# Kernel optimization log

Measured on AMD Instinct MI355X. Metric: run time of the kernel, lower is better.

## Reference

```python
import jax, jax.numpy as jnp
import numpy as np


def _gru_cell(x, h, Wih, Whh, bih, bhh):
    # torch nn.GRU cell math: gates ordered [r, z, n]
    gi = Wih @ x + bih
    gh = Whh @ h + bhh
    ir, iz, inn = jnp.split(gi, 3)
    hr, hz, hn = jnp.split(gh, 3)
    r = jax.nn.sigmoid(ir + hr)
    z = jax.nn.sigmoid(iz + hz)
    n = jnp.tanh(inn + r * hn)
    return (1.0 - z) * n + z * h


def _lrelu(x):
    # torch nn.LeakyReLU default negative_slope=0.01
    return jnp.where(x >= 0, x, 0.01 * x)


def setup_inputs() -> dict:
    key = jax.random.key(0)
    ks = jax.random.split(key, 24)
    V, E, H, C, S, T = 32000, 512, 1024, 2048, 256, 129
    w = lambda k, shape: jax.random.normal(k, shape, jnp.float32) * 0.02
    return {
        "inputs": jax.random.randint(ks[0], (T,), 0, V),
        "h1": jax.random.normal(ks[1], (H,), jnp.float32),
        "h2": jax.random.normal(ks[2], (H,), jnp.float32),
        "projected_keys": jax.random.normal(ks[3], (S, H), jnp.float32),
        "encoder_outputs": jax.random.normal(ks[4], (S, C), jnp.float32),
        "embeds": jax.random.normal(ks[5], (V, E), jnp.float32),
        "Wq": w(ks[6], (H, H)),
        "v_att": w(ks[7], (H,)),
        "W_ih1": w(ks[8], (3 * H, E + C)),
        "W_hh1": w(ks[9], (3 * H, H)),
        "b_ih1": w(ks[10], (3 * H,)),
        "b_hh1": w(ks[11], (3 * H,)),
        "W_ih2": w(ks[12], (3 * H, H + C)),
        "W_hh2": w(ks[13], (3 * H, H)),
        "b_ih2": w(ks[14], (3 * H,)),
        "b_hh2": w(ks[15], (3 * H,)),
        "W_pre": w(ks[16], (H, E + H + C)),
        "b_pre": w(ks[17], (H,)),
        "W_out": w(ks[18], (E, H)),
        "b_out": w(ks[19], (E,)),
    }


def reference(inputs, h1, h2, projected_keys, encoder_outputs, embeds, Wq, v_att,
              W_ih1, W_hh1, b_ih1, b_hh1, W_ih2, W_hh2, b_ih2, b_hh2,
              W_pre, b_pre, W_out, b_out):
    # teacher_forcing = 1.0 -> decoder input at step i is inputs[i] (ground truth)
    emb_seq = embeds[inputs[:-1]]  # [T-1, E]

    def step(carry, emb):
        h1, h2 = carry
        # additive attention: query from top-layer hidden state
        q = Wq @ h2                                     # [H]
        e = jnp.tanh(projected_keys + q) @ v_att        # [S]
        alphas = jax.nn.softmax(e)                      # [S]
        context = alphas @ encoder_outputs              # [C]
        h1n = _gru_cell(jnp.concatenate([emb, context]), h1, W_ih1, W_hh1, b_ih1, b_hh1)
        o1 = _lrelu(h1n)                                # dropout identity (eval)
        h2n = _gru_cell(jnp.concatenate([o1, context]), h2, W_ih2, W_hh2, b_ih2, b_hh2)
        o2 = _lrelu(h2n)
        pre = _lrelu(W_pre @ jnp.concatenate([emb, o2, context]) + b_pre)  # [H]
        out = W_out @ o2 + b_out                        # [E]
        return (h1n, h2n), (out, pre, alphas)

    (h1f, h2f), (outs, pres, alphas) = jax.lax.scan(step, (h1, h2), emb_seq)
    # torch.cat(outputs, dim=1) of [1,1,E] pieces -> [1, T-1, E]
    return outs[None], pres[None], alphas, h1f, h2f
```

## Files before the change

kernel.cpp:

```cpp
#include <hip/hip_runtime.h>
#include <hip/hip_bf16.h>

typedef unsigned int uint32;
typedef unsigned short ushort16;

#define GBLK 256
#define BT 512
#define NSTEP 128

#define OFF_WQ    0ull
#define OFF_WHH1  1048576ull
#define OFF_WHH2  4194304ull
#define OFF_WIH1  7340032ull
#define OFF_WIH2  15204352ull
#define OFF_WPRE  24641536ull
#define OFF_WOUT  28311552ull
#define OFF_PK    28835840ull
#define OFF_ENC   29097984ull
#define CONV_TOTAL 29622272ull

struct Params {
  const int* inputs;
  const float *h1_in, *h2_in, *embeds, *vatt;
  const void *pk, *enc, *Wq, *Wih1, *Whh1, *Wih2, *Whh2, *Wpre, *Wout;
  const float *bih1, *bhh1, *bih2, *bhh2, *bpre, *bout;
  float* out;
  float* ws;
  int* bar;
  int cw;
};

__device__ __forceinline__ float blo(uint32 u) { return __uint_as_float(u << 16); }
__device__ __forceinline__ float bhi(uint32 u) { return __uint_as_float(u & 0xffff0000u); }
__device__ __forceinline__ uint32 bfr(float f) {
  uint32 u = __float_as_uint(f);
  return (u + 0x7fffu + ((u >> 16) & 1u)) >> 16;
}

__device__ __forceinline__ float ald(const float* a) {
  return __hip_atomic_load(a, __ATOMIC_RELAXED, __HIP_MEMORY_SCOPE_AGENT);
}
__device__ __forceinline__ void ast(float* a, float v) {
  __hip_atomic_store(a, v, __ATOMIC_RELAXED, __HIP_MEMORY_SCOPE_AGENT);
}

__device__ __forceinline__ float wsum(float v) {
#pragma unroll
  for (int o = 32; o; o >>= 1) v += __shfl_xor(v, o, 64);
  return v;
}

template <bool CW>
__device__ __forceinline__ float rowchunk(const void* W, size_t base, const float* xc, int lane) {
  const float* x = xc + lane * 8;
  float4 x0 = *(const float4*)x, x1 = *(const float4*)(x + 4);
  if constexpr (CW) {
    uint4 w = *(const uint4*)((const ushort16*)W + base + lane * 8);
    return blo(w.x) * x0.x + bhi(w.x) * x0.y + blo(w.y) * x0.z + bhi(w.y) * x0.w +
           blo(w.z) * x1.x + bhi(w.z) * x1.y + blo(w.w) * x1.z + bhi(w.w) * x1.w;
  } else {
    const float* wf = (const float*)W + base + lane * 8;
    float4 w0 = *(const float4*)wf, w1 = *(const float4*)(wf + 4);
    return w0.x * x0.x + w0.y * x0.y + w0.z * x0.z + w0.w * x0.w +
           w1.x * x1.x + w1.y * x1.y + w1.z * x1.z + w1.w * x1.w;
  }
}

template <bool CW, int K>
__device__ __forceinline__ float rowdot(const void* W, size_t rowbase, const float* x, int lane) {
  float s = 0.f;
#pragma unroll
  for (int c = 0; c < K; c += 512) s += rowchunk<CW>(W, rowbase + c, x + c, lane);
  return wsum(s);
}

__device__ __forceinline__ void gbar(int* bar, int k) {
  __syncthreads();
  if (threadIdx.x == 0) {
    const int grp = blockIdx.x >> 4;
    int* gcnt = bar + grp * 32;
    int* grel = bar + 512 + grp * 32;
    int* rcnt = bar + 1024;
    int* rrel = bar + 1056;
    int v = __hip_atomic_fetch_add(gcnt, 1, __ATOMIC_RELEASE, __HIP_MEMORY_SCOPE_AGENT);
    if (v == k * 16 - 1) {
      int r = __hip_atomic_fetch_add(rcnt, 1, __ATOMIC_RELEASE, __HIP_MEMORY_SCOPE_AGENT);
      if (r == k * 16 - 1)
        __hip_atomic_store(rrel, k, __ATOMIC_RELAXED, __HIP_MEMORY_SCOPE_AGENT);
      while (__hip_atomic_load(rrel, __ATOMIC_RELAXED, __HIP_MEMORY_SCOPE_AGENT) < k)
        __builtin_amdgcn_s_sleep(1);
      __hip_atomic_store(grel, k, __ATOMIC_RELAXED, __HIP_MEMORY_SCOPE_AGENT);
    } else {
      while (__hip_atomic_load(grel, __ATOMIC_RELAXED, __HIP_MEMORY_SCOPE_AGENT) < k)
        __builtin_amdgcn_s_sleep(1);
    }
  }
  __syncthreads();
}

__device__ __forceinline__ float sigm(float x) { return 1.f / (1.f + expf(-x)); }
__device__ __forceinline__ float lrelu(float x) { return x >= 0.f ? x : 0.01f * x; }

__device__ __forceinline__ void conv_arr(const float* src, ushort16* dst, int n, int g) {
  for (int i = g * 4; i < n; i += GBLK * BT * 4) {
    float4 v = *(const float4*)(src + i);
    uint2 o;
    o.x = bfr(v.x) | (bfr(v.y) << 16);
    o.y = bfr(v.z) | (bfr(v.w) << 16);
    *(uint2*)(dst + i) = o;
  }
}

template <bool CW>
__device__ void run_decoder(const Params& p, float* sx, float* s_red, float* s_part) {
  const int tid = threadIdx.x;
  const int lane = tid & 63;
  const int w = tid >> 6;
  const int b = blockIdx.x;
  const int gw = b * 8 + w;

  float* h1w = p.ws + 2048;
  float* h2w = p.ws + 3072;
  float* qw = p.ws + 4096;
  float* evw = p.ws + 5120;
  float* ctxw = p.ws + 5376;
  float* o1w = p.ws + 7424;
  float* o2w = p.ws + 8448;
  float* gh1 = p.ws + 9472;
  float* gh2 = p.ws + 12544;

  ushort16* cb = (ushort16*)((char*)p.ws + 65536);
  const void* Wqc = CW ? (const void*)(cb + OFF_WQ) : p.Wq;
  const void* Whh1c = CW ? (const void*)(cb + OFF_WHH1) : p.Whh1;
  const void* Whh2c = CW ? (const void*)(cb + OFF_WHH2) : p.Whh2;
  const void* Wih1c = CW ? (const void*)(cb + OFF_WIH1) : p.Wih1;
  const void* Wih2c = CW ? (const void*)(cb + OFF_WIH2) : p.Wih2;
  const void* Wprec = CW ? (const void*)(cb + OFF_WPRE) : p.Wpre;
  const void* Woutc = CW ? (const void*)(cb + OFF_WOUT) : p.Wout;
  const void* pkc = CW ? (const void*)(cb + OFF_PK) : p.pk;
  const void* encc = CW ? (const void*)(cb + OFF_ENC) : p.enc;

  float* outs = p.out;
  float* pres = p.out + 65536;
  float* alph = p.out + 196608;
  float* h1f = p.out + 229376;
  float* h2f = p.out + 230400;

  if constexpr (CW) {
    const int g = b * BT + tid;
    conv_arr((const float*)p.Wq, cb + OFF_WQ, 1048576, g);
    conv_arr((const float*)p.Whh1, cb + OFF_WHH1, 3145728, g);
    conv_arr((const float*)p.Whh2, cb + OFF_WHH2, 3145728, g);
    conv_arr((const float*)p.Wih1, cb + OFF_WIH1, 7864320, g);
    conv_arr((const float*)p.Wih2, cb + OFF_WIH2, 9437184, g);
    conv_arr((const float*)p.Wpre, cb + OFF_WPRE, 3670016, g);
    conv_arr((const float*)p.Wout, cb + OFF_WOUT, 524288, g);
    conv_arr((const float*)p.pk, cb + OFF_PK, 262144, g);
    conv_arr((const float*)p.enc, cb + OFF_ENC, 524288, g);
  }
  if (gw < 16) ast(h1w + gw * 64 + lane, p.h1_in[gw * 64 + lane]);
  else if (gw < 32) ast(h2w + (gw - 16) * 64 + lane, p.h2_in[(gw - 16) * 64 + lane]);

  int bk = 0;
  gbar(p.bar, ++bk);

  for (int t = 0; t <= NSTEP; ++t) {
    gbar(p.bar, ++bk);
    {
      const float* embp = p.embeds + (size_t)p.inputs[t > 0 ? t - 1 : 0] * 512;
      for (int i = tid; i < 5632; i += BT) {
        float v;
        if (i < 512) v = embp[i];
        else if (i < 1536) v = ald(o2w + i - 512);
        else if (i < 3584) v = ald(ctxw + i - 1536);
        else if (i < 4608) v = ald(h1w + i - 3584);
        else v = ald(h2w + i - 4608);
        sx[i] = v;
      }
      __syncthreads();
      if (gw < 1024) {
        if (t > 0) {
          float s = rowdot<CW, 3584>(Wprec, (size_t)gw * 3584, sx, lane);
          if (lane == 0) pres[(size_t)(t - 1) * 1024 + gw] = lrelu(s + p.bpre[gw]);
        }
        for (int j = gw; j < 2048; j += 1024) {
          float s = rowdot<CW, 1024>(Whh1c, (size_t)j * 1024, sx + 3584, lane);
          if (lane == 0) ast(gh1 + j, s + p.bhh1[j]);
        }
      } else {
        for (int j = 2048 + (gw - 1024); j < 7680; j += 1024) {
          if (j < 3072) {
            float s = rowdot<CW, 1024>(Whh1c, (size_t)j * 1024, sx + 3584, lane);
            if (lane == 0) ast(gh1 + j, s + p.bhh1[j]);
          } else if (j < 6144) {
            int r = j - 3072;
            float s = rowdot<CW, 1024>(Whh2c, (size_t)r * 1024, sx + 4608, lane);
            if (lane == 0) ast(gh2 + r, s + p.bhh2[r]);
          } else if (j < 7168) {
            int r = j - 6144;
            float s = rowdot<CW, 1024>(Wqc, (size_t)r * 1024, sx + 4608, lane);
            if (lane == 0) ast(qw + r, s);
          } else if (t > 0) {
            int r = j - 7168;
            float s = rowdot<CW, 1024>(Woutc, (size_t)r * 1024, sx + 512, lane);
            if (lane == 0) outs[(size_t)(t - 1) * 512 + r] = s + p.bout[r];
          }
        }
      }
    }
    if (t == NSTEP) break;

    gbar(p.bar, ++bk);
    if (w == 0) {
      const int base = lane * 16;
      float pkv[16], qv[16], vv[16];
      if constexpr (CW) {
        const uint4* pp = (const uint4*)((const ushort16*)pkc + (size_t)b * 1024 + base);
        uint4 a = pp[0], c = pp[1];
        pkv[0] = blo(a.x); pkv[1] = bhi(a.x); pkv[2] = blo(a.y); pkv[3] = bhi(a.y);
        pkv[4] = blo(a.z); pkv[5] = bhi(a.z); pkv[6] = blo(a.w); pkv[7] = bhi(a.w);
        pkv[8] = blo(c.x); pkv[9] = bhi(c.x); pkv[10] = blo(c.y); pkv[11] = bhi(c.y);
        pkv[12] = blo(c.z); pkv[13] = bhi(c.z); pkv[14] = blo(c.w); pkv[15] = bhi(c.w);
      } else {
#pragma unroll
        for (int k = 0; k < 4; ++k)
          *(float4*)(pkv + k * 4) = *(const float4*)((const float*)pkc + (size_t)b * 1024 + base + k * 4);
      }
#pragma unroll
      for (int k = 0; k < 16; ++k) qv[k] = ald(qw + base + k);
#pragma unroll
      for (int k = 0; k < 4; ++k)
        *(float4*)(vv + k * 4) = *(const float4*)(p.vatt + base + k * 4);
      float acc = 0.f;
#pragma unroll
      for (int k = 0; k < 16; ++k) acc += tanhf(pkv[k] + qv[k]) * vv[k];
      acc = wsum(acc);
      if (lane == 0) ast(evw + b, acc);
    }

    gbar(p.bar, ++bk);
    {
      float e_i = 0.f, pe = 0.f;
      if (tid < 256) {
        e_i = ald(evw + tid);
        float mw = e_i;
#pragma unroll
        for (int o = 32; o; o >>= 1) mw = fmaxf(mw, __shfl_xor(mw, o, 64));
        if (lane == 0) s_red[w] = mw;
      }
      __syncthreads();
      float m = fmaxf(fmaxf(s_red[0], s_red[1]), fmaxf(s_red[2], s_red[3]));
      __syncthreads();
      if (tid < 256) {
        pe = expf(e_i - m);
        float zw = wsum(pe);
        if (lane == 0) s_red[w] = zw;
      }
      __syncthreads();
      float Z = s_red[0] + s_red[1] + s_red[2] + s_red[3];
      const int j0 = b * 8;
      if (tid < 256) {
        float alpha = pe / Z;
        if (b == 0) alph[(size_t)t * 256 + tid] = alpha;
        float c[8];
        if constexpr (CW) {
          uint4 wv = *(const uint4*)((const ushort16*)encc + (size_t)tid * 2048 + j0);
          c[0] = blo(wv.x); c[1] = bhi(wv.x); c[2] = blo(wv.y); c[3] = bhi(wv.y);
          c[4] = blo(wv.z); c[5] = bhi(wv.z); c[6] = blo(wv.w); c[7] = bhi(wv.w);
        } else {
          const float* er = (const float*)encc + (size_t)tid * 2048 + j0;
          *(float4*)c = *(const float4*)er;
          *(float4*)(c + 4) = *(const float4*)(er + 4);
        }
#pragma unroll
        for (int j = 0; j < 8; ++j) sx[tid * 8 + j] = alpha * c[j];
      }
      __syncthreads();
      for (int st = 128; st >= 1; st >>= 1) {
        if (tid < st) {
#pragma unroll
          for (int j = 0; j < 8; ++j) sx[tid * 8 + j] += sx[(tid + st) * 8 + j];
        }
        __syncthreads();
      }
      if (tid < 8) ast(ctxw + j0 + tid, sx[tid]);
    }

    gbar(p.bar, ++bk);
    {
      const float* embc = p.embeds + (size_t)p.inputs[t] * 512;
      for (int i = tid; i < 2560; i += BT)
        sx[i] = (i < 512) ? embc[i] : ald(ctxw + i - 512);
      __syncthreads();
      const int i0 = b * 4;
      for (int mm = w; mm < 60; mm += 8) {
        int r = mm / 15, m = mm % 15;
        int g = m / 5, c = m % 5;
        int row = g * 1024 + i0 + r;
        float s = rowchunk<CW>(Wih1c, (size_t)row * 2560 + c * 512, sx + c * 512, lane);
        s = wsum(s);
        if (lane == 0) s_part[mm] = s;
      }
      __syncthreads();
      if (tid < 4) {
        const int i = i0 + tid;
        const float* sp = s_part + tid * 15;
        float sr = sp[0] + sp[1] + sp[2] + sp[3] + sp[4];
        float sz = sp[5] + sp[6] + sp[7] + sp[8] + sp[9];
        float sn = sp[10] + sp[11] + sp[12] + sp[13] + sp[14];
        float r = sigm(sr + p.bih1[i] + ald(gh1 + i));
        float z = sigm(sz + p.bih1[1024 + i] + ald(gh1 + 1024 + i));
        float n = tanhf(sn + p.bih1[2048 + i] + r * ald(gh1 + 2048 + i));
        float h = (1.f - z) * n + z * ald(h1w + i);
        ast(h1w + i, h);
        ast(o1w + i, lrelu(h));
      }
    }

    gbar(p.bar, ++bk);
    {
      for (int i = tid; i < 3072; i += BT)
        sx[i] = (i < 1024) ? ald(o1w + i) : ald(ctxw + i - 1024);
      __syncthreads();
      const int i0 = b * 4;
      for (int mm = w; mm < 72; mm += 8) {
        int r = mm / 18, m = mm % 18;
        int g = m / 6, c = m % 6;
        int row = g * 1024 + i0 + r;
        float s = rowchunk<CW>(Wih2c, (size_t)row * 3072 + c * 512, sx + c * 512, lane);
        s = wsum(s);
        if (lane == 0) s_part[mm] = s;
      }
      __syncthreads();
      if (tid < 4) {
        const int i = i0 + tid;
        const float* sp = s_part + tid * 18;
        float sr = sp[0] + sp[1] + sp[2] + sp[3] + sp[4] + sp[5];
        float sz = sp[6] + sp[7] + sp[8] + sp[9] + sp[10] + sp[11];
        float sn = sp[12] + sp[13] + sp[14] + sp[15] + sp[16] + sp[17];
        float r = sigm(sr + p.bih2[i] + ald(gh2 + i));
        float z = sigm(sz + p.bih2[1024 + i] + ald(gh2 + 1024 + i));
        float n = tanhf(sn + p.bih2[2048 + i] + r * ald(gh2 + 2048 + i));
        float h = (1.f - z) * n + z * ald(h2w + i);
        ast(h2w + i, h);
        ast(o2w + i, lrelu(h));
      }
    }
  }
  if (gw < 16) h1f[gw * 64 + lane] = ald(h1w + gw * 64 + lane);
  else if (gw < 32) h2f[(gw - 16) * 64 + lane] = ald(h2w + (gw - 16) * 64 + lane);
}

__global__ __launch_bounds__(BT, 2) void dec_SAVE_30683246363209_kernel(Params p) {
  __shared__ float sx[5632];
  __shared__ float s_red[8];
  __shared__ float s_part[72];
  if (p.cw) run_decoder<true>(p, sx, s_red, s_part);
  else run_decoder<false>(p, sx, s_red, s_part);
}

extern "C" void kernel_launch(void* const* d_in, const int* in_sizes, int n_in,
                              void* d_out, int out_size, void* d_ws, size_t ws_size,
                              hipStream_t stream) {
  hipMemsetAsync(d_ws, 0, 65536, stream);

  Params p;
  p.inputs = (const int*)d_in[0];
  p.h1_in = (const float*)d_in[1];
  p.h2_in = (const float*)d_in[2];
  p.pk = d_in[3];
  p.enc = d_in[4];
  p.embeds = (const float*)d_in[5];
  p.Wq = d_in[6];
  p.vatt = (const float*)d_in[7];
  p.Wih1 = d_in[8];
  p.Whh1 = d_in[9];
  p.bih1 = (const float*)d_in[10];
  p.bhh1 = (const float*)d_in[11];
  p.Wih2 = d_in[12];
  p.Whh2 = d_in[13];
  p.bih2 = (const float*)d_in[14];
  p.bhh2 = (const float*)d_in[15];
  p.Wpre = d_in[16];
  p.bpre = (const float*)d_in[17];
  p.Wout = d_in[18];
  p.bout = (const float*)d_in[19];
  p.out = (float*)d_out;
  p.ws = (float*)d_ws;
  p.bar = (int*)d_ws;
  p.cw = (ws_size >= (size_t)(65536 + CONV_TOTAL * 2)) ? 1 : 0;

  void* args[] = {&p};
  hipError_t err = hipLaunchCooperativeKernel((const void*)dec_SAVE_30683246363209_kernel,
                                              dim3(GBLK), dim3(BT), args, 0, stream);
  if (err != hipSuccess) {
    dec_SAVE_30683246363209_kernel<<<dim3(GBLK), dim3(BT), 0, stream>>>(p);
  }
}
```

Measured before the change: 6.865 ms.

## Keep all weights resident in registers as packed bf16 across decoder steps

Drops the global bf16 conversion pass into workspace. Each wave now loads its fixed weight rows once, converts them to packed bf16 and keeps them in registers (about 120 dwords per thread) for all 129 steps. The aim is to remove the per-step weight streaming from HBM/L2 that dominated each timestep. The attention energy is also spread across the whole block with an 8-wave reduction instead of running on one wave. The cost is heavy register pressure at 512 threads with 2 blocks per CU, which risks spills or losing occupancy, and the cooperative launch needs every block resident.

```diff
diff --git a/kernel.cpp b/kernel.cpp
--- a/kernel.cpp
+++ b/kernel.cpp
@@ -1,33 +1,19 @@
 #include <hip/hip_runtime.h>
-#include <hip/hip_bf16.h>
 
 typedef unsigned int uint32;
-typedef unsigned short ushort16;
 
 #define GBLK 256
 #define BT 512
 #define NSTEP 128
 
-#define OFF_WQ    0ull
-#define OFF_WHH1  1048576ull
-#define OFF_WHH2  4194304ull
-#define OFF_WIH1  7340032ull
-#define OFF_WIH2  15204352ull
-#define OFF_WPRE  24641536ull
-#define OFF_WOUT  28311552ull
-#define OFF_PK    28835840ull
-#define OFF_ENC   29097984ull
-#define CONV_TOTAL 29622272ull
-
 struct Params {
   const int* inputs;
   const float *h1_in, *h2_in, *embeds, *vatt;
-  const void *pk, *enc, *Wq, *Wih1, *Whh1, *Wih2, *Whh2, *Wpre, *Wout;
+  const float *pk, *enc, *Wq, *Wih1, *Whh1, *Wih2, *Whh2, *Wpre, *Wout;
   const float *bih1, *bhh1, *bih2, *bhh2, *bpre, *bout;
   float* out;
   float* ws;
   int* bar;
-  int cw;
 };
 
 __device__ __forceinline__ float blo(uint32 u) { return __uint_as_float(u << 16); }
@@ -50,28 +36,21 @@
   return v;
 }
 
-template <bool CW>
-__device__ __forceinline__ float rowchunk(const void* W, size_t base, const float* xc, int lane) {
+__device__ __forceinline__ void ldchunk(const float* W, size_t base, int lane, uint32* r) {
+  const float* wf = W + base + lane * 8;
+  float4 a = *(const float4*)wf;
+  float4 c = *(const float4*)(wf + 4);
+  r[0] = bfr(a.x) | (bfr(a.y) << 16);
+  r[1] = bfr(a.z) | (bfr(a.w) << 16);
+  r[2] = bfr(c.x) | (bfr(c.y) << 16);
+  r[3] = bfr(c.z) | (bfr(c.w) << 16);
+}
+
+__device__ __forceinline__ float dotchunk(const uint32* r, const float* xc, int lane) {
   const float* x = xc + lane * 8;
   float4 x0 = *(const float4*)x, x1 = *(const float4*)(x + 4);
-  if constexpr (CW) {
-    uint4 w = *(const uint4*)((const ushort16*)W + base + lane * 8);
-    return blo(w.x) * x0.x + bhi(w.x) * x0.y + blo(w.y) * x0.z + bhi(w.y) * x0.w +
-           blo(w.z) * x1.x + bhi(w.z) * x1.y + blo(w.w) * x1.z + bhi(w.w) * x1.w;
-  } else {
-    const float* wf = (const float*)W + base + lane * 8;
-    float4 w0 = *(const float4*)wf, w1 = *(const float4*)(wf + 4);
-    return w0.x * x0.x + w0.y * x0.y + w0.z * x0.z + w0.w * x0.w +
-           w1.x * x1.x + w1.y * x1.y + w1.z * x1.z + w1.w * x1.w;
-  }
-}
-
-template <bool CW, int K>
-__device__ __forceinline__ float rowdot(const void* W, size_t rowbase, const float* x, int lane) {
-  float s = 0.f;
-#pragma unroll
-  for (int c = 0; c < K; c += 512) s += rowchunk<CW>(W, rowbase + c, x + c, lane);
-  return wsum(s);
+  return blo(r[0]) * x0.x + bhi(r[0]) * x0.y + blo(r[1]) * x0.z + bhi(r[1]) * x0.w +
+         blo(r[2]) * x1.x + bhi(r[2]) * x1.y + blo(r[3]) * x1.z + bhi(r[3]) * x1.w;
 }
 
 __device__ __forceinline__ void gbar(int* bar, int k) {
@@ -101,23 +80,18 @@
 __device__ __forceinline__ float sigm(float x) { return 1.f / (1.f + expf(-x)); }
 __device__ __forceinline__ float lrelu(float x) { return x >= 0.f ? x : 0.01f * x; }
 
-__device__ __forceinline__ void conv_arr(const float* src, ushort16* dst, int n, int g) {
-  for (int i = g * 4; i < n; i += GBLK * BT * 4) {
-    float4 v = *(const float4*)(src + i);
-    uint2 o;
-    o.x = bfr(v.x) | (bfr(v.y) << 16);
-    o.y = bfr(v.z) | (bfr(v.w) << 16);
-    *(uint2*)(dst + i) = o;
-  }
-}
-
-template <bool CW>
-__device__ void run_decoder(const Params& p, float* sx, float* s_red, float* s_part) {
+__global__ __launch_bounds__(BT, 2) void dec_regw_kernel(Params p) {
+  __shared__ float sx[5632];
+  __shared__ float s_red[8];
+  __shared__ float s_part[72];
+
   const int tid = threadIdx.x;
   const int lane = tid & 63;
   const int w = tid >> 6;
   const int b = blockIdx.x;
   const int gw = b * 8 + w;
+  const int i0 = b * 4;
+  const int j0 = b * 8;
 
   float* h1w = p.ws + 2048;
   float* h2w = p.ws + 3072;
@@ -129,35 +103,71 @@
   float* gh1 = p.ws + 9472;
   float* gh2 = p.ws + 12544;
 
-  ushort16* cb = (ushort16*)((char*)p.ws + 65536);
-  const void* Wqc = CW ? (const void*)(cb + OFF_WQ) : p.Wq;
-  const void* Whh1c = CW ? (const void*)(cb + OFF_WHH1) : p.Whh1;
-  const void* Whh2c = CW ? (const void*)(cb + OFF_WHH2) : p.Whh2;
-  const void* Wih1c = CW ? (const void*)(cb + OFF_WIH1) : p.Wih1;
-  const void* Wih2c = CW ? (const void*)(cb + OFF_WIH2) : p.Wih2;
-  const void* Wprec = CW ? (const void*)(cb + OFF_WPRE) : p.Wpre;
-  const void* Woutc = CW ? (const void*)(cb + OFF_WOUT) : p.Wout;
-  const void* pkc = CW ? (const void*)(cb + OFF_PK) : p.pk;
-  const void* encc = CW ? (const void*)(cb + OFF_ENC) : p.enc;
-
   float* outs = p.out;
   float* pres = p.out + 65536;
   float* alph = p.out + 196608;
   float* h1f = p.out + 229376;
   float* h2f = p.out + 230400;
 
-  if constexpr (CW) {
-    const int g = b * BT + tid;
-    conv_arr((const float*)p.Wq, cb + OFF_WQ, 1048576, g);
-    conv_arr((const float*)p.Whh1, cb + OFF_WHH1, 3145728, g);
-    conv_arr((const float*)p.Whh2, cb + OFF_WHH2, 3145728, g);
-    conv_arr((const float*)p.Wih1, cb + OFF_WIH1, 7864320, g);
-    conv_arr((const float*)p.Wih2, cb + OFF_WIH2, 9437184, g);
-    conv_arr((const float*)p.Wpre, cb + OFF_WPRE, 3670016, g);
-    conv_arr((const float*)p.Wout, cb + OFF_WOUT, 524288, g);
-    conv_arr((const float*)p.pk, cb + OFF_PK, 262144, g);
-    conv_arr((const float*)p.enc, cb + OFF_ENC, 524288, g);
-  }
+  uint32 wa[48];
+  if (gw < 1024) {
+#pragma unroll
+    for (int c = 0; c < 7; ++c)
+      ldchunk(p.Wpre, (size_t)gw * 3584 + c * 512, lane, wa + 4 * c);
+    ldchunk(p.Whh1, (size_t)gw * 1024, lane, wa + 28);
+    ldchunk(p.Whh1, (size_t)gw * 1024 + 512, lane, wa + 32);
+    ldchunk(p.Whh1, (size_t)(gw + 1024) * 1024, lane, wa + 36);
+    ldchunk(p.Whh1, (size_t)(gw + 1024) * 1024 + 512, lane, wa + 40);
+    wa[44] = wa[45] = wa[46] = wa[47] = 0u;
+  } else {
+    const int widx = gw - 1024;
+    ldchunk(p.Whh1, (size_t)(2048 + widx) * 1024, lane, wa + 0);
+    ldchunk(p.Whh1, (size_t)(2048 + widx) * 1024 + 512, lane, wa + 4);
+#pragma unroll
+    for (int r = 0; r < 3; ++r) {
+      ldchunk(p.Whh2, (size_t)(widx + r * 1024) * 1024, lane, wa + 8 + 8 * r);
+      ldchunk(p.Whh2, (size_t)(widx + r * 1024) * 1024 + 512, lane, wa + 12 + 8 * r);
+    }
+    ldchunk(p.Wq, (size_t)widx * 1024, lane, wa + 32);
+    ldchunk(p.Wq, (size_t)widx * 1024 + 512, lane, wa + 36);
+    const int wr = widx & 511;
+    ldchunk(p.Wout, (size_t)wr * 1024, lane, wa + 40);
+    ldchunk(p.Wout, (size_t)wr * 1024 + 512, lane, wa + 44);
+  }
+
+  uint32 wd[32];
+#pragma unroll
+  for (int k = 0; k < 8; ++k) {
+    const int mm = w + 8 * k;
+    const int mmc = mm < 60 ? mm : 0;
+    const int r = mmc / 15, m = mmc % 15, g = m / 5, c = m % 5;
+    ldchunk(p.Wih1, (size_t)(g * 1024 + i0 + r) * 2560 + c * 512, lane, wd + 4 * k);
+  }
+
+  uint32 we9[36];
+#pragma unroll
+  for (int k = 0; k < 9; ++k) {
+    const int mm = w + 8 * k;
+    const int r = mm / 18, m = mm % 18, g = m / 6, c = m % 6;
+    ldchunk(p.Wih2, (size_t)(g * 1024 + i0 + r) * 3072 + c * 512, lane, we9 + 4 * k);
+  }
+
+  uint32 wenc[4] = {0u, 0u, 0u, 0u};
+  if (tid < 256) {
+    const float* er = p.enc + (size_t)tid * 2048 + j0;
+    float4 a = *(const float4*)er, c = *(const float4*)(er + 4);
+    wenc[0] = bfr(a.x) | (bfr(a.y) << 16);
+    wenc[1] = bfr(a.z) | (bfr(a.w) << 16);
+    wenc[2] = bfr(c.x) | (bfr(c.y) << 16);
+    wenc[3] = bfr(c.z) | (bfr(c.w) << 16);
+  }
+
+  const int d0 = tid * 2;
+  const float pk0 = p.pk[(size_t)b * 1024 + d0];
+  const float pk1 = p.pk[(size_t)b * 1024 + d0 + 1];
+  const float va0 = p.vatt[d0];
+  const float va1 = p.vatt[d0 + 1];
+
   if (gw < 16) ast(h1w + gw * 64 + lane, p.h1_in[gw * 64 + lane]);
   else if (gw < 32) ast(h2w + (gw - 16) * 64 + lane, p.h2_in[(gw - 16) * 64 + lane]);
 
@@ -180,62 +190,54 @@
       __syncthreads();
       if (gw < 1024) {
         if (t > 0) {
-          float s = rowdot<CW, 3584>(Wprec, (size_t)gw * 3584, sx, lane);
+          float s = 0.f;
+#pragma unroll
+          for (int c = 0; c < 7; ++c) s += dotchunk(wa + 4 * c, sx + 512 * c, lane);
+          s = wsum(s);
           if (lane == 0) pres[(size_t)(t - 1) * 1024 + gw] = lrelu(s + p.bpre[gw]);
         }
-        for (int j = gw; j < 2048; j += 1024) {
-          float s = rowdot<CW, 1024>(Whh1c, (size_t)j * 1024, sx + 3584, lane);
-          if (lane == 0) ast(gh1 + j, s + p.bhh1[j]);
-        }
+        float s1 = dotchunk(wa + 28, sx + 3584, lane) + dotchunk(wa + 32, sx + 4096, lane);
+        s1 = wsum(s1);
+        if (lane == 0) ast(gh1 + gw, s1 + p.bhh1[gw]);
+        float s2 = dotchunk(wa + 36, sx + 3584, lane) + dotchunk(wa + 40, sx + 4096, lane);
+        s2 = wsum(s2);
+        if (lane == 0) ast(gh1 + 1024 + gw, s2 + p.bhh1[1024 + gw]);
       } else {
-        for (int j = 2048 + (gw - 1024); j < 7680; j += 1024) {
-          if (j < 3072) {
-            float s = rowdot<CW, 1024>(Whh1c, (size_t)j * 1024, sx + 3584, lane);
-            if (lane == 0) ast(gh1 + j, s + p.bhh1[j]);
-          } else if (j < 6144) {
-            int r = j - 3072;
-            float s = rowdot<CW, 1024>(Whh2c, (size_t)r * 1024, sx + 4608, lane);
-            if (lane == 0) ast(gh2 + r, s + p.bhh2[r]);
-          } else if (j < 7168) {
-            int r = j - 6144;
-            float s = rowdot<CW, 1024>(Wqc, (size_t)r * 1024, sx + 4608, lane);
-            if (lane == 0) ast(qw + r, s);
-          } else if (t > 0) {
-            int r = j - 7168;
-            float s = rowdot<CW, 1024>(Woutc, (size_t)r * 1024, sx + 512, lane);
-            if (lane == 0) outs[(size_t)(t - 1) * 512 + r] = s + p.bout[r];
-          }
+        const int widx = gw - 1024;
+        float s = dotchunk(wa + 0, sx + 3584, lane) + dotchunk(wa + 4, sx + 4096, lane);
+        s = wsum(s);
+        if (lane == 0) ast(gh1 + 2048 + widx, s + p.bhh1[2048 + widx]);
+#pragma unroll
+        for (int r = 0; r < 3; ++r) {
+          float t2 = dotchunk(wa + 8 + 8 * r, sx + 4608, lane) +
+                     dotchunk(wa + 12 + 8 * r, sx + 5120, lane);
+          t2 = wsum(t2);
+          if (lane == 0) ast(gh2 + widx + 1024 * r, t2 + p.bhh2[widx + 1024 * r]);
+        }
+        float sq = dotchunk(wa + 32, sx + 4608, lane) + dotchunk(wa + 36, sx + 5120, lane);
+        sq = wsum(sq);
+        if (lane == 0) ast(qw + widx, sq);
+        if (t > 0 && widx < 512) {
+          float so = dotchunk(wa + 40, sx + 512, lane) + dotchunk(wa + 44, sx + 1024, lane);
+          so = wsum(so);
+          if (lane == 0) outs[(size_t)(t - 1) * 512 + widx] = so + p.bout[widx];
         }
       }
     }
     if (t == NSTEP) break;
 
     gbar(p.bar, ++bk);
-    if (w == 0) {
-      const int base = lane * 16;
-      float pkv[16], qv[16], vv[16];
-      if constexpr (CW) {
-        const uint4* pp = (const uint4*)((const ushort16*)pkc + (size_t)b * 1024 + base);
-        uint4 a = pp[0], c = pp[1];
-        pkv[0] = blo(a.x); pkv[1] = bhi(a.x); pkv[2] = blo(a.y); pkv[3] = bhi(a.y);
-        pkv[4] = blo(a.z); pkv[5] = bhi(a.z); pkv[6] = blo(a.w); pkv[7] = bhi(a.w);
-        pkv[8] = blo(c.x); pkv[9] = bhi(c.x); pkv[10] = blo(c.y); pkv[11] = bhi(c.y);
-        pkv[12] = blo(c.z); pkv[13] = bhi(c.z); pkv[14] = blo(c.w); pkv[15] = bhi(c.w);
-      } else {
-#pragma unroll
-        for (int k = 0; k < 4; ++k)
-          *(float4*)(pkv + k * 4) = *(const float4*)((const float*)pkc + (size_t)b * 1024 + base + k * 4);
-      }
-#pragma unroll
-      for (int k = 0; k < 16; ++k) qv[k] = ald(qw + base + k);
-#pragma unroll
-      for (int k = 0; k < 4; ++k)
-        *(float4*)(vv + k * 4) = *(const float4*)(p.vatt + base + k * 4);
-      float acc = 0.f;
-#pragma unroll
-      for (int k = 0; k < 16; ++k) acc += tanhf(pkv[k] + qv[k]) * vv[k];
+    {
+      float q0 = ald(qw + d0), q1 = ald(qw + d0 + 1);
+      float acc = va0 * tanhf(pk0 + q0) + va1 * tanhf(pk1 + q1);
       acc = wsum(acc);
-      if (lane == 0) ast(evw + b, acc);
+      if (lane == 0) s_red[w] = acc;
+      __syncthreads();
+      if (tid == 0) {
+        float e = s_red[0] + s_red[1] + s_red[2] + s_red[3] +
+                  s_red[4] + s_red[5] + s_red[6] + s_red[7];
+        ast(evw + b, e);
+      }
     }
 
     gbar(p.bar, ++bk);
@@ -258,22 +260,17 @@
       }
       __syncthreads();
       float Z = s_red[0] + s_red[1] + s_red[2] + s_red[3];
-      const int j0 = b * 8;
       if (tid < 256) {
         float alpha = pe / Z;
         if (b == 0) alph[(size_t)t * 256 + tid] = alpha;
-        float c[8];
-        if constexpr (CW) {
-          uint4 wv = *(const uint4*)((const ushort16*)encc + (size_t)tid * 2048 + j0);
-          c[0] = blo(wv.x); c[1] = bhi(wv.x); c[2] = blo(wv.y); c[3] = bhi(wv.y);
-          c[4] = blo(wv.z); c[5] = bhi(wv.z); c[6] = blo(wv.w); c[7] = bhi(wv.w);
-        } else {
-          const float* er = (const float*)encc + (size_t)tid * 2048 + j0;
-          *(float4*)c = *(const float4*)er;
-          *(float4*)(c + 4) = *(const float4*)(er + 4);
-        }
-#pragma unroll
-        for (int j = 0; j < 8; ++j) sx[tid * 8 + j] = alpha * c[j];
+        sx[tid * 8 + 0] = alpha * blo(wenc[0]);
+        sx[tid * 8 + 1] = alpha * bhi(wenc[0]);
+        sx[tid * 8 + 2] = alpha * blo(wenc[1]);
+        sx[tid * 8 + 3] = alpha * bhi(wenc[1]);
+        sx[tid * 8 + 4] = alpha * blo(wenc[2]);
+        sx[tid * 8 + 5] = alpha * bhi(wenc[2]);
+        sx[tid * 8 + 6] = alpha * blo(wenc[3]);
+        sx[tid * 8 + 7] = alpha * bhi(wenc[3]);
       }
       __syncthreads();
       for (int st = 128; st >= 1; st >>= 1) {
@@ -292,14 +289,15 @@
       for (int i = tid; i < 2560; i += BT)
         sx[i] = (i < 512) ? embc[i] : ald(ctxw + i - 512);
       __syncthreads();
-      const int i0 = b * 4;
-      for (int mm = w; mm < 60; mm += 8) {
-        int r = mm / 15, m = mm % 15;
-        int g = m / 5, c = m % 5;
-        int row = g * 1024 + i0 + r;
-        float s = rowchunk<CW>(Wih1c, (size_t)row * 2560 + c * 512, sx + c * 512, lane);
-        s = wsum(s);
-        if (lane == 0) s_part[mm] = s;
+#pragma unroll
+      for (int k = 0; k < 8; ++k) {
+        const int mm = w + 8 * k;
+        if (mm < 60) {
+          const int c = (mm % 15) % 5;
+          float s = dotchunk(wd + 4 * k, sx + c * 512, lane);
+          s = wsum(s);
+          if (lane == 0) s_part[mm] = s;
+        }
       }
       __syncthreads();
       if (tid < 4) {
@@ -322,12 +320,11 @@
       for (int i = tid; i < 3072; i += BT)
         sx[i] = (i < 1024) ? ald(o1w + i) : ald(ctxw + i - 1024);
       __syncthreads();
-      const int i0 = b * 4;
-      for (int mm = w; mm < 72; mm += 8) {
-        int r = mm / 18, m = mm % 18;
-        int g = m / 6, c = m % 6;
-        int row = g * 1024 + i0 + r;
-        float s = rowchunk<CW>(Wih2c, (size_t)row * 3072 + c * 512, sx + c * 512, lane);
+#pragma unroll
+      for (int k = 0; k < 9; ++k) {
+        const int mm = w + 8 * k;
+        const int c = (mm % 18) % 6;
+        float s = dotchunk(we9 + 4 * k, sx + c * 512, lane);
         s = wsum(s);
         if (lane == 0) s_part[mm] = s;
       }
@@ -351,14 +348,6 @@
   else if (gw < 32) h2f[(gw - 16) * 64 + lane] = ald(h2w + (gw - 16) * 64 + lane);
 }
 
-__global__ __launch_bounds__(BT, 2) void dec_SAVE_30683246363209_kernel(Params p) {
-  __shared__ float sx[5632];
-  __shared__ float s_red[8];
-  __shared__ float s_part[72];
-  if (p.cw) run_decoder<true>(p, sx, s_red, s_part);
-  else run_decoder<false>(p, sx, s_red, s_part);
-}
-
 extern "C" void kernel_launch(void* const* d_in, const int* in_sizes, int n_in,
                               void* d_out, int out_size, void* d_ws, size_t ws_size,
                               hipStream_t stream) {
@@ -368,32 +357,31 @@
   p.inputs = (const int*)d_in[0];
   p.h1_in = (const float*)d_in[1];
   p.h2_in = (const float*)d_in[2];
-  p.pk = d_in[3];
-  p.enc = d_in[4];
+  p.pk = (const float*)d_in[3];
+  p.enc = (const float*)d_in[4];
   p.embeds = (const float*)d_in[5];
-  p.Wq = d_in[6];
+  p.Wq = (const float*)d_in[6];
   p.vatt = (const float*)d_in[7];
-  p.Wih1 = d_in[8];
-  p.Whh1 = d_in[9];
+  p.Wih1 = (const float*)d_in[8];
+  p.Whh1 = (const float*)d_in[9];
   p.bih1 = (const float*)d_in[10];
   p.bhh1 = (const float*)d_in[11];
-  p.Wih2 = d_in[12];
-  p.Whh2 = d_in[13];
+  p.Wih2 = (const float*)d_in[12];
+  p.Whh2 = (const float*)d_in[13];
   p.bih2 = (const float*)d_in[14];
   p.bhh2 = (const float*)d_in[15];
-  p.Wpre = d_in[16];
+  p.Wpre = (const float*)d_in[16];
   p.bpre = (const float*)d_in[17];
-  p.Wout = d_in[18];
+  p.Wout = (const float*)d_in[18];
   p.bout = (const float*)d_in[19];
   p.out = (float*)d_out;
   p.ws = (float*)d_ws;
   p.bar = (int*)d_ws;
-  p.cw = (ws_size >= (size_t)(65536 + CONV_TOTAL * 2)) ? 1 : 0;
 
   void* args[] = {&p};
-  hipError_t err = hipLaunchCooperativeKernel((const void*)dec_SAVE_30683246363209_kernel,
+  hipError_t err = hipLaunchCooperativeKernel((const void*)dec_regw_kernel,
                                               dim3(GBLK), dim3(BT), args, 0, stream);
   if (err != hipSuccess) {
-    dec_SAVE_30683246363209_kernel<<<dim3(GBLK), dim3(BT), 0, stream>>>(p);
-  }
-}
+    dec_regw_kernel<<<dim3(GBLK), dim3(BT), 0, stream>>>(p);
+  }
+}
```

Measured after the change: 7.239 ms. 1.05x slower.
